# Optimization experiments

Measured on AMD Instinct MI355X. Metric: run time of the kernel, lower is better.

The kernel has to match this reference:

```python
import jax, jax.numpy as jnp
import numpy as np

N_WORDS = 30000
EMB_DIM = 784
MAT_DIM = 28  # sqrt(784)
BATCH = 1024
SEQ = 64


def setup_inputs() -> dict:
    key = jax.random.key(0)
    k_sent, k_w = jax.random.split(key)
    sent = jax.random.randint(k_sent, (BATCH, SEQ), 0, N_WORDS + 1, dtype=jnp.int64 if jax.config.jax_enable_x64 else jnp.int32)
    # cmow 'identity' init: N(0, 0.1) + flattened identity; row 0 is the neutral element (identity matrix)
    eye_flat = jnp.eye(MAT_DIM, dtype=jnp.float32).reshape(1, EMB_DIM)
    init_w = 0.1 * jax.random.normal(k_w, (N_WORDS, EMB_DIM), dtype=jnp.float32) + eye_flat
    table = jnp.concatenate([eye_flat, init_w], axis=0)  # [N_WORDS+1, 784]
    return {"sent": sent, "table": table}


def reference(sent, table):
    B, S = sent.shape
    # embedding lookup, view as per-word matrices: [B, S, 28, 28]
    mats = table[sent].reshape(B, S, MAT_DIM, MAT_DIM)
    # left-to-right matrix chain product: cur = cur @ mats[:, i]
    def step(carry, m):
        return jnp.matmul(carry, m), None
    # seq-major for scan: [S-1, B, 28, 28]
    rest = jnp.swapaxes(mats[:, 1:], 0, 1)
    prod, _ = jax.lax.scan(step, mats[:, 0], rest)
    return prod.reshape(B, EMB_DIM)  # flatten matrix -> [B, 784]
```

## Files before the change

### kernel.cpp

```cpp
#include <hip/hip_runtime.h>
#include <hip/hip_bf16.h>


#define MD    28
#define MD2   784
#define SEQL  64
#define CHUNK 16

typedef __attribute__((ext_vector_type(8))) short bf16x8;
typedef __attribute__((ext_vector_type(4))) float floatx4;

#define LDS_FENCE() asm volatile("s_waitcnt lgkmcnt(0)" ::: "memory")

__device__ __forceinline__ unsigned short f2bf(float x) {
    unsigned u = __float_as_uint(x);
    unsigned r = u + 0x7FFFu + ((u >> 16) & 1u);
    return (unsigned short)(r >> 16);
}
__device__ __forceinline__ float bf2f(unsigned short h) {
    return __uint_as_float(((unsigned)h) << 16);
}

__device__ __forceinline__ unsigned pk_bf16(float x, float y) {
    float2 f; f.x = x; f.y = y;
    __hip_bfloat162 h2 = __float22bfloat162_rn(f);
    union { __hip_bfloat162 h; unsigned u; } cv; cv.h = h2;
    return cv.u;
}

union U4F { uint4 u; bf16x8 v; };

__device__ __forceinline__ void pack8(const float* v, bf16x8* hi, bf16x8* lo) {
    U4F H, L;
    unsigned* ph = (unsigned*)&H.u;
    unsigned* pl = (unsigned*)&L.u;
    #pragma unroll
    for (int p = 0; p < 4; ++p) {
        float x = v[2*p], y = v[2*p+1];
        unsigned h = pk_bf16(x, y);
        float rx = x - __uint_as_float(h << 16);
        float ry = y - __uint_as_float(h & 0xffff0000u);
        pl[p] = pk_bf16(rx, ry);
        ph[p] = h;
    }
    *hi = H.v; *lo = L.v;
}

__device__ __forceinline__ int xaddr(int n, int g, int h) {
    return n * 64 + ((h ^ (n & 1)) << 5) + ((g ^ ((n >> 1) & 3)) << 3);
}

struct Acc { floatx4 t[2][2]; };

__device__ __forceinline__ void acc_zero(Acc& a) {
    #pragma unroll
    for (int mi = 0; mi < 2; ++mi)
        #pragma unroll
        for (int ni = 0; ni < 2; ++ni)
            a.t[mi][ni] = (floatx4){0.f, 0.f, 0.f, 0.f};
}

__device__ __forceinline__ floatx4 mfma16(bf16x8 a, bf16x8 b, floatx4 c) {
    return __builtin_amdgcn_mfma_f32_16x16x32_bf16(a, b, c, 0, 0, 0);
}

__device__ __forceinline__ void mm12(bf16x8 ah0, bf16x8 ah1, bf16x8 al0, bf16x8 al1,
                                     bf16x8 bh0, bf16x8 bh1, bf16x8 bl0, bf16x8 bl1,
                                     Acc& acc) {
    acc.t[0][0] = mfma16(ah0, bh0, acc.t[0][0]);
    acc.t[0][1] = mfma16(ah0, bh1, acc.t[0][1]);
    acc.t[1][0] = mfma16(ah1, bh0, acc.t[1][0]);
    acc.t[1][1] = mfma16(ah1, bh1, acc.t[1][1]);
    acc.t[0][0] = mfma16(ah0, bl0, acc.t[0][0]);
    acc.t[0][1] = mfma16(ah0, bl1, acc.t[0][1]);
    acc.t[1][0] = mfma16(ah1, bl0, acc.t[1][0]);
    acc.t[1][1] = mfma16(ah1, bl1, acc.t[1][1]);
    acc.t[0][0] = mfma16(al0, bh0, acc.t[0][0]);
    acc.t[0][1] = mfma16(al0, bh1, acc.t[0][1]);
    acc.t[1][0] = mfma16(al1, bh0, acc.t[1][0]);
    acc.t[1][1] = mfma16(al1, bh1, acc.t[1][1]);
}

__device__ __forceinline__ void readB(const unsigned short* X, int n16, int q,
                                      bf16x8* bh0, bf16x8* bh1, bf16x8* bl0, bf16x8* bl1) {
    *bh0 = *(const bf16x8*)(X + xaddr(n16,      q, 0));
    *bl0 = *(const bf16x8*)(X + xaddr(n16,      q, 1));
    *bh1 = *(const bf16x8*)(X + xaddr(16 + n16, q, 0));
    *bl1 = *(const bf16x8*)(X + xaddr(16 + n16, q, 1));
}

__device__ __forceinline__ void writeX(unsigned short* X, const Acc& acc,
                                       int n16, int q) {
    const int sub = (q & 1) * 4;
    #pragma unroll
    for (int mi = 0; mi < 2; ++mi) {
        const int g = 2 * mi + (q >> 1);
        #pragma unroll
        for (int ni = 0; ni < 2; ++ni) {
            floatx4 a = acc.t[mi][ni];
            const int n = ni * 16 + n16;
            unsigned h0 = pk_bf16(a[0], a[1]);
            unsigned h1 = pk_bf16(a[2], a[3]);
            float r0 = a[0] - __uint_as_float(h0 << 16);
            float r1 = a[1] - __uint_as_float(h0 & 0xffff0000u);
            float r2 = a[2] - __uint_as_float(h1 << 16);
            float r3 = a[3] - __uint_as_float(h1 & 0xffff0000u);
            unsigned l0 = pk_bf16(r0, r1);
            unsigned l1 = pk_bf16(r2, r3);
            uint2 uh; uh.x = h0; uh.y = h1;
            uint2 ul; ul.x = l0; ul.y = l1;
            *(uint2*)(X + xaddr(n, g, 0) + sub) = uh;
            *(uint2*)(X + xaddr(n, g, 1) + sub) = ul;
        }
    }
}

__device__ __forceinline__ void writeA_scratch(unsigned short* S, const Acc& acc,
                                               int n16, int q) {
    unsigned short* Sh = S;
    unsigned short* Sl = S + 1024;
    #pragma unroll
    for (int mi = 0; mi < 2; ++mi)
        #pragma unroll
        for (int ni = 0; ni < 2; ++ni) {
            floatx4 a = acc.t[mi][ni];
            #pragma unroll
            for (int r = 0; r < 4; ++r) {
                int m = mi * 16 + q * 4 + r;
                int n = ni * 16 + n16;
                int off = m * 32 + n;
                unsigned short hh = f2bf(a[r]);
                Sh[off] = hh;
                Sl[off] = f2bf(a[r] - bf2f(hh));
            }
        }
}

__device__ __forceinline__ void readA_scratch(const unsigned short* S, int n16, int q,
                                              bf16x8* ah0, bf16x8* ah1,
                                              bf16x8* al0, bf16x8* al1) {
    const unsigned short* Sh = S;
    const unsigned short* Sl = S + 1024;
    const int o0 = n16 * 32 + 8 * q;
    const int o1 = (16 + n16) * 32 + 8 * q;
    *ah0 = *(const bf16x8*)(Sh + o0);
    *ah1 = *(const bf16x8*)(Sh + o1);
    *al0 = *(const bf16x8*)(Sl + o0);
    *al1 = *(const bf16x8*)(Sl + o1);
}

__device__ __forceinline__ void prefA(const float* __restrict__ Mg, int n16, int q,
                                      float* pa, float* pb) {
    const bool bok = (n16 < MD - 16);
    #pragma unroll
    for (int j = 0; j < 8; ++j) {
        int k = 8 * q + j;
        bool kv = (k < MD);
        pa[j] = kv ? Mg[k * MD + n16] : 0.f;
        pb[j] = (kv && bok) ? Mg[k * MD + 16 + n16] : 0.f;
    }
}

__global__ __launch_bounds__(256, 4)
void cmow_mfma_kernel(const int* __restrict__ sent,
                      const float* __restrict__ table,
                      float* __restrict__ out)
{
    __shared__ __align__(16) unsigned short smem[12288];

    const int tid  = threadIdx.x;
    const int lane = tid & 63;
    const int w    = tid >> 6;
    const int b    = blockIdx.x;

    unsigned short* Xw = smem + w * 2048;

    const int* sp = sent + b * SEQL + w * CHUNK;
    int idx[CHUNK];
    #pragma unroll
    for (int i = 0; i < CHUNK; ++i) idx[i] = sp[i];

    const int n16 = lane & 15;
    const int q   = lane >> 4;

    {
        const int nr = lane & 31;
        const int h2 = lane >> 5;
        float v[16];
        #pragma unroll
        for (int t = 0; t < 16; ++t) v[t] = 0.f;
        if (nr < MD) {
            const float* src = table + (size_t)idx[0] * MD2 + nr * MD + 16 * h2;
            const int nval = (h2 == 0) ? 16 : 12;
            #pragma unroll
            for (int t = 0; t < 16; t += 4) {
                if (t < nval) {
                    float4 f = *(const float4*)(src + t);
                    v[t] = f.x; v[t+1] = f.y; v[t+2] = f.z; v[t+3] = f.w;
                }
            }
        }
        #pragma unroll
        for (int s = 0; s < 2; ++s) {
            bf16x8 hi, lo;
            pack8(v + 8 * s, &hi, &lo);
            int g = 2 * h2 + s;
            *(bf16x8*)(Xw + xaddr(nr, g, 0)) = hi;
            *(bf16x8*)(Xw + xaddr(nr, g, 1)) = lo;
        }
    }

    float pa[8], pb[8];
    prefA(table + (size_t)idx[1] * MD2, n16, q, pa, pb);
    LDS_FENCE();

    for (int i = 1; i < CHUNK; ++i) {
        bf16x8 ah0, ah1, al0, al1;
        pack8(pa, &ah0, &al0);
        pack8(pb, &ah1, &al1);
        if (i + 1 < CHUNK)
            prefA(table + (size_t)idx[i + 1] * MD2, n16, q, pa, pb);

        bf16x8 bh0, bh1, bl0, bl1;
        readB(Xw, n16, q, &bh0, &bh1, &bl0, &bl1);

        Acc acc; acc_zero(acc);
        mm12(ah0, ah1, al0, al1, bh0, bh1, bl0, bl1, acc);

        if (i < CHUNK - 1 || (w & 1) == 0)
            writeX(Xw, acc, n16, q);
        else
            writeA_scratch(smem + 8192 + (w >> 1) * 2048, acc, n16, q);
        LDS_FENCE();
    }

    __syncthreads();

    if (w < 2) {
        bf16x8 ah0, ah1, al0, al1, bh0, bh1, bl0, bl1;
        readA_scratch(smem + 8192 + w * 2048, n16, q, &ah0, &ah1, &al0, &al1);
        readB(smem + (2 * w) * 2048, n16, q, &bh0, &bh1, &bl0, &bl1);
        Acc acc; acc_zero(acc);
        mm12(ah0, ah1, al0, al1, bh0, bh1, bl0, bl1, acc);
        if (w == 0) writeX(smem, acc, n16, q);
        else        writeA_scratch(smem + 8192 + 2048, acc, n16, q);
    }
    __syncthreads();

    if (w == 0) {
        bf16x8 ah0, ah1, al0, al1, bh0, bh1, bl0, bl1;
        readA_scratch(smem + 8192 + 2048, n16, q, &ah0, &ah1, &al0, &al1);
        readB(smem, n16, q, &bh0, &bh1, &bl0, &bl1);
        Acc acc; acc_zero(acc);
        mm12(ah0, ah1, al0, al1, bh0, bh1, bl0, bl1, acc);

        float* op = out + (size_t)b * MD2;
        #pragma unroll
        for (int mi = 0; mi < 2; ++mi)
            #pragma unroll
            for (int ni = 0; ni < 2; ++ni) {
                int C = ni * 16 + n16;
                int R = mi * 16 + q * 4;
                if (C < MD && R + 3 < MD) {
                    floatx4 a = acc.t[mi][ni];
                    float4 st; st.x = a[0]; st.y = a[1]; st.z = a[2]; st.w = a[3];
                    *(float4*)(op + C * MD + R) = st;
                }
            }
    }
}

extern "C" void kernel_launch(void* const* d_in, const int* in_sizes, int n_in,
                              void* d_out, int out_size, void* d_ws, size_t ws_size,
                              hipStream_t stream) {
    const int*   sent  = (const int*)d_in[0];
    const float* table = (const float*)d_in[1];
    float*       outp  = (float*)d_out;

    const int batch = in_sizes[0] / SEQL;
    cmow_mfma_kernel<<<dim3(batch), dim3(256), 0, stream>>>(sent, table, outp);
}
```

Before: 174.5 us.

## Split each sequence across eight waves with a three-level tree reduction

Each block now uses 512 threads (8 waves), and each wave chains 8 word matrices instead of 16. The partial products are then combined in a three-level tree reduction in LDS (4, then 2, then 1 wave). Odd waves write their result in A-operand layout into their own LDS slot, which removes the separate scratch region. This shortens the serial dependent chain per wave, at the cost of more sync levels and larger blocks that may reduce how many blocks fit per CU.

```diff
diff --git a/kernel.cpp b/kernel.cpp
--- a/kernel.cpp
+++ b/kernel.cpp
@@ -5,7 +5,8 @@
 #define MD    28
 #define MD2   784
 #define SEQL  64
-#define CHUNK 16
+#define CHUNK 8
+#define WPB   8
 
 typedef __attribute__((ext_vector_type(8))) short bf16x8;
 typedef __attribute__((ext_vector_type(4))) float floatx4;
@@ -115,10 +116,10 @@
     }
 }
 
-__device__ __forceinline__ void writeA_scratch(unsigned short* S, const Acc& acc,
-                                               int n16, int q) {
-    unsigned short* Sh = S;
-    unsigned short* Sl = S + 1024;
+__device__ __forceinline__ void writeAconv(unsigned short* P, const Acc& acc,
+                                           int n16, int q) {
+    unsigned short* Sh = P;
+    unsigned short* Sl = P + 1024;
     #pragma unroll
     for (int mi = 0; mi < 2; ++mi)
         #pragma unroll
@@ -136,11 +137,11 @@
         }
 }
 
-__device__ __forceinline__ void readA_scratch(const unsigned short* S, int n16, int q,
-                                              bf16x8* ah0, bf16x8* ah1,
-                                              bf16x8* al0, bf16x8* al1) {
-    const unsigned short* Sh = S;
-    const unsigned short* Sl = S + 1024;
+__device__ __forceinline__ void readAconv(const unsigned short* P, int n16, int q,
+                                          bf16x8* ah0, bf16x8* ah1,
+                                          bf16x8* al0, bf16x8* al1) {
+    const unsigned short* Sh = P;
+    const unsigned short* Sl = P + 1024;
     const int o0 = n16 * 32 + 8 * q;
     const int o1 = (16 + n16) * 32 + 8 * q;
     *ah0 = *(const bf16x8*)(Sh + o0);
@@ -161,12 +162,12 @@
     }
 }
 
-__global__ __launch_bounds__(256, 4)
+__global__ __launch_bounds__(512, 8)
 void cmow_mfma_kernel(const int* __restrict__ sent,
                       const float* __restrict__ table,
                       float* __restrict__ out)
 {
-    __shared__ __align__(16) unsigned short smem[12288];
+    __shared__ __align__(16) unsigned short smem[WPB * 2048];
 
     const int tid  = threadIdx.x;
     const int lane = tid & 63;
@@ -230,26 +231,37 @@
         if (i < CHUNK - 1 || (w & 1) == 0)
             writeX(Xw, acc, n16, q);
         else
-            writeA_scratch(smem + 8192 + (w >> 1) * 2048, acc, n16, q);
+            writeAconv(Xw, acc, n16, q);
         LDS_FENCE();
     }
 
+    __syncthreads();
+
+    if (w < 4) {
+        bf16x8 ah0, ah1, al0, al1, bh0, bh1, bl0, bl1;
+        readAconv(smem + (2 * w + 1) * 2048, n16, q, &ah0, &ah1, &al0, &al1);
+        readB(smem + (2 * w) * 2048, n16, q, &bh0, &bh1, &bl0, &bl1);
+        Acc acc; acc_zero(acc);
+        mm12(ah0, ah1, al0, al1, bh0, bh1, bl0, bl1, acc);
+        if ((w & 1) == 0) writeX(smem + (2 * w) * 2048, acc, n16, q);
+        else              writeAconv(smem + (2 * w + 1) * 2048, acc, n16, q);
+    }
     __syncthreads();
 
     if (w < 2) {
         bf16x8 ah0, ah1, al0, al1, bh0, bh1, bl0, bl1;
-        readA_scratch(smem + 8192 + w * 2048, n16, q, &ah0, &ah1, &al0, &al1);
-        readB(smem + (2 * w) * 2048, n16, q, &bh0, &bh1, &bl0, &bl1);
+        readAconv(smem + (4 * w + 3) * 2048, n16, q, &ah0, &ah1, &al0, &al1);
+        readB(smem + (4 * w) * 2048, n16, q, &bh0, &bh1, &bl0, &bl1);
         Acc acc; acc_zero(acc);
         mm12(ah0, ah1, al0, al1, bh0, bh1, bl0, bl1, acc);
         if (w == 0) writeX(smem, acc, n16, q);
-        else        writeA_scratch(smem + 8192 + 2048, acc, n16, q);
+        else        writeAconv(smem + 7 * 2048, acc, n16, q);
     }
     __syncthreads();
 
     if (w == 0) {
         bf16x8 ah0, ah1, al0, al1, bh0, bh1, bl0, bl1;
-        readA_scratch(smem + 8192 + 2048, n16, q, &ah0, &ah1, &al0, &al1);
+        readAconv(smem + 7 * 2048, n16, q, &ah0, &ah1, &al0, &al1);
         readB(smem, n16, q, &bh0, &bh1, &bl0, &bl1);
         Acc acc; acc_zero(acc);
         mm12(ah0, ah1, al0, al1, bh0, bh1, bl0, bl1, acc);
@@ -278,5 +290,5 @@
     float*       outp  = (float*)d_out;
 
     const int batch = in_sizes[0] / SEQL;
-    cmow_mfma_kernel<<<dim3(batch), dim3(256), 0, stream>>>(sent, table, outp);
-}
+    cmow_mfma_kernel<<<dim3(batch), dim3(512), 0, stream>>>(sent, table, outp);
+}
```

Measured after the change: 672.9 us. 3.86x slower.
